# Kernel optimization log

Measured on AMD Instinct MI355X. Metric: run time of the kernel, lower is better.

## Reference

```python
import jax, jax.numpy as jnp
import numpy as np

HIDDEN = 4096


def setup_inputs() -> dict:
    key = jax.random.key(0)
    k1, k2 = jax.random.split(key)
    hidden_states = jax.random.normal(k1, (8, 2048, HIDDEN), dtype=jnp.float32)
    # gate_proj ~ N(0, 0.02^2), shape (2*hidden, hidden)
    gate_proj = 0.02 * jax.random.normal(k2, (2 * HIDDEN, HIDDEN), dtype=jnp.float32)
    return {"hidden_states": hidden_states, "gate_proj": gate_proj, "world_size": 8}


def reference(hidden_states, gate_proj, world_size):
    h = gate_proj.shape[1]
    view = hidden_states.reshape(-1, h)                 # [N, h]
    mm = jnp.einsum("nh,oh->no", view, gate_proj)      # [N, 2h]  (x @ W.T)
    n, o = mm.shape
    # reduce-scatter over dim 0 with world_size ranks: sum the per-rank chunks
    out = mm.reshape(world_size, n // world_size, o).sum(axis=0)  # [N/W, 2h]
    return out
```

## Files before the change

kernel.cpp:

```cpp
#include <hip/hip_runtime.h>
#include <hip/hip_bf16.h>


#define HID   4096
#define SEQ   2048
#define WORLD 8
#define OUTD  8192

typedef __bf16 bf16x8 __attribute__((ext_vector_type(8)));
typedef short  s16x8  __attribute__((ext_vector_type(8)));
typedef float  f32x4  __attribute__((ext_vector_type(4)));

typedef const __attribute__((address_space(1))) void* gas1_ptr;
typedef __attribute__((address_space(3))) void*       las3_ptr;

static __device__ __forceinline__ unsigned short f2bf(float f) {
    union { float f; unsigned u; } v; v.f = f;
    unsigned u = v.u;
    u += 0x7fffu + ((u >> 16) & 1u);
    return (unsigned short)(u >> 16);
}

__global__ void reduce_x_kernel(const float* __restrict__ hs,
                                unsigned short* __restrict__ xb) {
    const int total4 = SEQ * HID / 4;
    const float4* h4 = (const float4*)hs;
    ushort4* o4 = (ushort4*)xb;
    for (int i = blockIdx.x * blockDim.x + threadIdx.x; i < total4;
         i += gridDim.x * blockDim.x) {
        float4 s = h4[i];
        #pragma unroll
        for (int w = 1; w < WORLD; ++w) {
            float4 t = h4[i + w * total4];
            s.x += t.x; s.y += t.y; s.z += t.z; s.w += t.w;
        }
        ushort4 o;
        o.x = f2bf(s.x); o.y = f2bf(s.y); o.z = f2bf(s.z); o.w = f2bf(s.w);
        o4[i] = o;
    }
}

__global__ void convert_w_kernel(const float* __restrict__ w,
                                 unsigned short* __restrict__ wb) {
    const int total4 = OUTD * HID / 4;
    const float4* w4 = (const float4*)w;
    ushort4* o4 = (ushort4*)wb;
    for (int i = blockIdx.x * blockDim.x + threadIdx.x; i < total4;
         i += gridDim.x * blockDim.x) {
        float4 s = w4[i];
        ushort4 o;
        o.x = f2bf(s.x); o.y = f2bf(s.y); o.z = f2bf(s.z); o.w = f2bf(s.w);
        o4[i] = o;
    }
}


#define BM 256
#define BN 256
#define BK 64
#define KSTEPS (HID / BK)

__global__ __launch_bounds__(512, 2)
void gemm_bt_kernel(const unsigned short* __restrict__ A,
                    const unsigned short* __restrict__ B,
                    float* __restrict__ C) {
    __shared__ __align__(16) unsigned short lsA[2][BM * BK];
    __shared__ __align__(16) unsigned short lsB[2][BN * BK];

    const int tid  = threadIdx.x;
    const int lane = tid & 63;
    const int wave = tid >> 6;
    const int wm   = wave >> 2;
    const int wn   = wave & 3;

    const int bid    = blockIdx.x;
    const int tileid = (bid & 7) * 32 + (bid >> 3);
    const int bm = tileid >> 5;
    const int bn = tileid & 31;

    const int subrow = lane >> 3;
    const int slot   = lane & 7;
    const int scol   = (slot ^ subrow) * 8;
    const unsigned short* aBase =
        A + (size_t)(bm * BM + wave * 8 + subrow) * HID + scol;
    const unsigned short* bBase =
        B + (size_t)(bn * BN + wave * 8 + subrow) * HID + scol;
    const int ldsW = wave * 8 * BK;

#define ST_A(buf, ktv, l) __builtin_amdgcn_global_load_lds(                     \
        (gas1_ptr)(aBase + (size_t)(ktv) * BK + (size_t)(l) * 64 * HID),        \
        (las3_ptr)(&lsA[buf][(l) * 64 * BK + ldsW]), 16, 0, 0)
#define ST_B(buf, ktv, l) __builtin_amdgcn_global_load_lds(                     \
        (gas1_ptr)(bBase + (size_t)(ktv) * BK + (size_t)(l) * 64 * HID),        \
        (las3_ptr)(&lsB[buf][(l) * 64 * BK + ldsW]), 16, 0, 0)

    const int fr    = lane & 15;
    const int fq    = lane >> 4;
    const int axor  = fr & 7;
    const int koff0 = ((0 + fq) ^ axor) * 8;
    const int koff1 = ((4 + fq) ^ axor) * 8;
    const int aRowB = (wm * 128 + fr) * BK;
    const int bRowB = (wn * 64 + fr) * BK;

#define RD_A(dst, p, mm, koff) dst = __builtin_bit_cast(bf16x8,                 \
        *(const s16x8*)&lsA[p][aRowB + (mm) * 16 * BK + (koff)])
#define RD_B(dst, p, nn, koff) dst = __builtin_bit_cast(bf16x8,                 \
        *(const s16x8*)&lsB[p][bRowB + (nn) * 16 * BK + (koff)])

#define BARRIER() __builtin_amdgcn_s_barrier()
#define LGKM0()   asm volatile("s_waitcnt lgkmcnt(0)" ::: "memory")
#define VMC4()    asm volatile("s_waitcnt vmcnt(4)" ::: "memory")
#define VMC0()    asm volatile("s_waitcnt vmcnt(0)" ::: "memory")
#define PRIO1()   __builtin_amdgcn_s_setprio(1)
#define PRIO0()   __builtin_amdgcn_s_setprio(0)

    f32x4 acc[8][4] = {};
    bf16x8 va[4][2], vb[4][2];

    ST_A(0, 0, 0); ST_A(0, 0, 1); ST_A(0, 0, 2); ST_A(0, 0, 3);
    ST_B(0, 0, 0); ST_B(0, 0, 1); ST_B(0, 0, 2); ST_B(0, 0, 3);
    ST_A(1, 1, 0); ST_A(1, 1, 1); ST_A(1, 1, 2); ST_A(1, 1, 3);
    VMC4();
    BARRIER();

    for (int kt = 0; kt < KSTEPS; ++kt) {
        const int p = kt & 1;
        const int q = p ^ 1;
        const bool s1 = (kt + 1 < KSTEPS);
        const bool s2 = (kt + 2 < KSTEPS);

        RD_A(va[0][0], p, 0, koff0); RD_A(va[0][1], p, 0, koff1);
        RD_A(va[1][0], p, 1, koff0); RD_A(va[1][1], p, 1, koff1);
        RD_A(va[2][0], p, 2, koff0); RD_A(va[2][1], p, 2, koff1);
        RD_A(va[3][0], p, 3, koff0); RD_A(va[3][1], p, 3, koff1);
        RD_B(vb[0][0], p, 0, koff0); RD_B(vb[0][1], p, 0, koff1);
        RD_B(vb[1][0], p, 1, koff0); RD_B(vb[1][1], p, 1, koff1);
        if (s1) { ST_B(q, kt + 1, 0); ST_B(q, kt + 1, 1); }
        BARRIER();
        LGKM0();
        PRIO1();
        #pragma unroll
        for (int s = 0; s < 2; ++s)
            #pragma unroll
            for (int m = 0; m < 4; ++m)
                #pragma unroll
                for (int n = 0; n < 2; ++n)
                    acc[m][n] = __builtin_amdgcn_mfma_f32_16x16x32_bf16(
                        va[m][s], vb[n][s], acc[m][n], 0, 0, 0);
        PRIO0();
        BARRIER();

        RD_B(vb[2][0], p, 2, koff0); RD_B(vb[2][1], p, 2, koff1);
        RD_B(vb[3][0], p, 3, koff0); RD_B(vb[3][1], p, 3, koff1);
        if (s1) { ST_B(q, kt + 1, 2); ST_B(q, kt + 1, 3); }
        BARRIER();
        LGKM0();
        PRIO1();
        #pragma unroll
        for (int s = 0; s < 2; ++s)
            #pragma unroll
            for (int m = 0; m < 4; ++m)
                #pragma unroll
                for (int n = 0; n < 2; ++n)
                    acc[m][2 + n] = __builtin_amdgcn_mfma_f32_16x16x32_bf16(
                        va[m][s], vb[2 + n][s], acc[m][2 + n], 0, 0, 0);
        PRIO0();
        BARRIER();

        RD_A(va[0][0], p, 4, koff0); RD_A(va[0][1], p, 4, koff1);
        RD_A(va[1][0], p, 5, koff0); RD_A(va[1][1], p, 5, koff1);
        RD_A(va[2][0], p, 6, koff0); RD_A(va[2][1], p, 6, koff1);
        RD_A(va[3][0], p, 7, koff0); RD_A(va[3][1], p, 7, koff1);
        BARRIER();
        LGKM0();
        PRIO1();
        #pragma unroll
        for (int s = 0; s < 2; ++s)
            #pragma unroll
            for (int m = 0; m < 4; ++m)
                #pragma unroll
                for (int n = 0; n < 2; ++n)
                    acc[4 + m][n] = __builtin_amdgcn_mfma_f32_16x16x32_bf16(
                        va[m][s], vb[n][s], acc[4 + m][n], 0, 0, 0);
        PRIO0();
        BARRIER();

        if (s2) { ST_A(p, kt + 2, 0); ST_A(p, kt + 2, 1);
                  ST_A(p, kt + 2, 2); ST_A(p, kt + 2, 3); }
        BARRIER();
        PRIO1();
        #pragma unroll
        for (int s = 0; s < 2; ++s)
            #pragma unroll
            for (int m = 0; m < 4; ++m)
                #pragma unroll
                for (int n = 0; n < 2; ++n)
                    acc[4 + m][2 + n] = __builtin_amdgcn_mfma_f32_16x16x32_bf16(
                        va[m][s], vb[2 + n][s], acc[4 + m][2 + n], 0, 0, 0);
        PRIO0();
        if (s2) { VMC4(); } else { VMC0(); }
        BARRIER();
    }

    const long crow0 = (long)bm * BM + wm * 128 + fq * 4;
    const long ccol0 = (long)bn * BN + wn * 64 + fr;
    #pragma unroll
    for (int m = 0; m < 8; ++m)
        #pragma unroll
        for (int n = 0; n < 4; ++n)
            #pragma unroll
            for (int j = 0; j < 4; ++j)
                C[(crow0 + m * 16 + j) * OUTD + ccol0 + n * 16] = acc[m][n][j];
}

extern "C" void kernel_launch(void* const* d_in, const int* in_sizes, int n_in,
                              void* d_out, int out_size, void* d_ws, size_t ws_size,
                              hipStream_t stream) {
    const float* hs = (const float*)d_in[0];
    const float* w  = (const float*)d_in[1];
    float* out = (float*)d_out;

    unsigned short* xb = (unsigned short*)d_ws;
    unsigned short* wb = xb + (size_t)SEQ * HID;

    hipLaunchKernelGGL(reduce_x_kernel, dim3(2048), dim3(256), 0, stream, hs, xb);
    hipLaunchKernelGGL(convert_w_kernel, dim3(4096), dim3(256), 0, stream, w, wb);
    hipLaunchKernelGGL(gemm_bt_kernel, dim3((SEQ / BM) * (OUTD / BN)), dim3(512),
                       0, stream, xb, wb, out);
}
```

Baseline: 242.0 us.

## Merge prep kernels, remap tiles per XCD, prefetch B two stages ahead

The separate reduce and convert kernels are merged into one launch that splits its blocks between the two jobs, removing one launch and the gap between kernels. The GEMM maps tiles so that each XCD gets a contiguous 4x8 block of output tiles, which should improve L2 reuse of A and B rows. The main loop now reads all four B fragments up front, iterates over A in pairs of rows, and issues both the A and B global-to-LDS loads two k-steps ahead with a vmcnt(8) wait. The deeper prefetch hides more memory latency but keeps more loads in flight and changes register pressure.

```diff
diff --git a/kernel.cpp b/kernel.cpp
--- a/kernel.cpp
+++ b/kernel.cpp
@@ -21,36 +21,39 @@
     return (unsigned short)(u >> 16);
 }
 
-__global__ void reduce_x_kernel(const float* __restrict__ hs,
-                                unsigned short* __restrict__ xb) {
-    const int total4 = SEQ * HID / 4;
-    const float4* h4 = (const float4*)hs;
-    ushort4* o4 = (ushort4*)xb;
-    for (int i = blockIdx.x * blockDim.x + threadIdx.x; i < total4;
-         i += gridDim.x * blockDim.x) {
-        float4 s = h4[i];
-        #pragma unroll
-        for (int w = 1; w < WORLD; ++w) {
-            float4 t = h4[i + w * total4];
-            s.x += t.x; s.y += t.y; s.z += t.z; s.w += t.w;
+#define RED_BLOCKS  2048
+#define CONV_BLOCKS 4096
+__global__ void prep_kernel(const float* __restrict__ hs,
+                            const float* __restrict__ w,
+                            unsigned short* __restrict__ xb,
+                            unsigned short* __restrict__ wb) {
+    if (blockIdx.x < RED_BLOCKS) {
+        const int total4 = SEQ * HID / 4;
+        const float4* h4 = (const float4*)hs;
+        ushort4* o4 = (ushort4*)xb;
+        for (int i = blockIdx.x * blockDim.x + threadIdx.x; i < total4;
+             i += RED_BLOCKS * blockDim.x) {
+            float4 s = h4[i];
+            #pragma unroll
+            for (int ww = 1; ww < WORLD; ++ww) {
+                float4 t = h4[i + ww * total4];
+                s.x += t.x; s.y += t.y; s.z += t.z; s.w += t.w;
+            }
+            ushort4 o;
+            o.x = f2bf(s.x); o.y = f2bf(s.y); o.z = f2bf(s.z); o.w = f2bf(s.w);
+            o4[i] = o;
         }
-        ushort4 o;
-        o.x = f2bf(s.x); o.y = f2bf(s.y); o.z = f2bf(s.z); o.w = f2bf(s.w);
-        o4[i] = o;
-    }
-}
-
-__global__ void convert_w_kernel(const float* __restrict__ w,
-                                 unsigned short* __restrict__ wb) {
-    const int total4 = OUTD * HID / 4;
-    const float4* w4 = (const float4*)w;
-    ushort4* o4 = (ushort4*)wb;
-    for (int i = blockIdx.x * blockDim.x + threadIdx.x; i < total4;
-         i += gridDim.x * blockDim.x) {
-        float4 s = w4[i];
-        ushort4 o;
-        o.x = f2bf(s.x); o.y = f2bf(s.y); o.z = f2bf(s.z); o.w = f2bf(s.w);
-        o4[i] = o;
+    } else {
+        const int total4 = OUTD * HID / 4;
+        const float4* w4 = (const float4*)w;
+        ushort4* o4 = (ushort4*)wb;
+        for (int i = (blockIdx.x - RED_BLOCKS) * blockDim.x + threadIdx.x;
+             i < total4; i += CONV_BLOCKS * blockDim.x) {
+            float4 s = w4[i];
+            ushort4 o;
+            o.x = f2bf(s.x); o.y = f2bf(s.y); o.z = f2bf(s.z); o.w = f2bf(s.w);
+            o4[i] = o;
+        }
     }
 }
 
@@ -73,10 +76,11 @@
     const int wm   = wave >> 2;
     const int wn   = wave & 3;
 
-    const int bid    = blockIdx.x;
-    const int tileid = (bid & 7) * 32 + (bid >> 3);
-    const int bm = tileid >> 5;
-    const int bn = tileid & 31;
+    const int bid   = blockIdx.x;
+    const int xcd   = bid & 7;
+    const int local = bid >> 3;
+    const int bm = (xcd >> 2) * 4 + (local >> 3);
+    const int bn = (xcd & 3) * 8 + (local & 7);
 
     const int subrow = lane >> 3;
     const int slot   = lane & 7;
@@ -109,96 +113,95 @@
 
 #define BARRIER() __builtin_amdgcn_s_barrier()
 #define LGKM0()   asm volatile("s_waitcnt lgkmcnt(0)" ::: "memory")
-#define VMC4()    asm volatile("s_waitcnt vmcnt(4)" ::: "memory")
+#define VMC8()    asm volatile("s_waitcnt vmcnt(8)" ::: "memory")
 #define VMC0()    asm volatile("s_waitcnt vmcnt(0)" ::: "memory")
 #define PRIO1()   __builtin_amdgcn_s_setprio(1)
 #define PRIO0()   __builtin_amdgcn_s_setprio(0)
 
     f32x4 acc[8][4] = {};
-    bf16x8 va[4][2], vb[4][2];
+    bf16x8 va[2][2], va2[2][2], vb[4][2];
 
     ST_A(0, 0, 0); ST_A(0, 0, 1); ST_A(0, 0, 2); ST_A(0, 0, 3);
     ST_B(0, 0, 0); ST_B(0, 0, 1); ST_B(0, 0, 2); ST_B(0, 0, 3);
     ST_A(1, 1, 0); ST_A(1, 1, 1); ST_A(1, 1, 2); ST_A(1, 1, 3);
-    VMC4();
+    ST_B(1, 1, 0); ST_B(1, 1, 1); ST_B(1, 1, 2); ST_B(1, 1, 3);
+    VMC8();
     BARRIER();
 
     for (int kt = 0; kt < KSTEPS; ++kt) {
         const int p = kt & 1;
-        const int q = p ^ 1;
-        const bool s1 = (kt + 1 < KSTEPS);
-        const bool s2 = (kt + 2 < KSTEPS);
-
+        const bool st = (kt + 2 < KSTEPS);
+
+        RD_B(vb[0][0], p, 0, koff0); RD_B(vb[0][1], p, 0, koff1);
+        RD_B(vb[1][0], p, 1, koff0); RD_B(vb[1][1], p, 1, koff1);
+        RD_B(vb[2][0], p, 2, koff0); RD_B(vb[2][1], p, 2, koff1);
+        RD_B(vb[3][0], p, 3, koff0); RD_B(vb[3][1], p, 3, koff1);
         RD_A(va[0][0], p, 0, koff0); RD_A(va[0][1], p, 0, koff1);
         RD_A(va[1][0], p, 1, koff0); RD_A(va[1][1], p, 1, koff1);
-        RD_A(va[2][0], p, 2, koff0); RD_A(va[2][1], p, 2, koff1);
-        RD_A(va[3][0], p, 3, koff0); RD_A(va[3][1], p, 3, koff1);
-        RD_B(vb[0][0], p, 0, koff0); RD_B(vb[0][1], p, 0, koff1);
-        RD_B(vb[1][0], p, 1, koff0); RD_B(vb[1][1], p, 1, koff1);
-        if (s1) { ST_B(q, kt + 1, 0); ST_B(q, kt + 1, 1); }
         BARRIER();
         LGKM0();
         PRIO1();
         #pragma unroll
         for (int s = 0; s < 2; ++s)
             #pragma unroll
-            for (int m = 0; m < 4; ++m)
-                #pragma unroll
-                for (int n = 0; n < 2; ++n)
+            for (int m = 0; m < 2; ++m)
+                #pragma unroll
+                for (int n = 0; n < 4; ++n)
                     acc[m][n] = __builtin_amdgcn_mfma_f32_16x16x32_bf16(
                         va[m][s], vb[n][s], acc[m][n], 0, 0, 0);
         PRIO0();
         BARRIER();
 
-        RD_B(vb[2][0], p, 2, koff0); RD_B(vb[2][1], p, 2, koff1);
-        RD_B(vb[3][0], p, 3, koff0); RD_B(vb[3][1], p, 3, koff1);
-        if (s1) { ST_B(q, kt + 1, 2); ST_B(q, kt + 1, 3); }
+        RD_A(va[0][0], p, 2, koff0); RD_A(va[0][1], p, 2, koff1);
+        RD_A(va[1][0], p, 3, koff0); RD_A(va[1][1], p, 3, koff1);
+        if (st) { ST_B(p, kt + 2, 0); ST_B(p, kt + 2, 1);
+                  ST_B(p, kt + 2, 2); ST_B(p, kt + 2, 3); }
         BARRIER();
         LGKM0();
         PRIO1();
         #pragma unroll
         for (int s = 0; s < 2; ++s)
             #pragma unroll
-            for (int m = 0; m < 4; ++m)
-                #pragma unroll
-                for (int n = 0; n < 2; ++n)
-                    acc[m][2 + n] = __builtin_amdgcn_mfma_f32_16x16x32_bf16(
-                        va[m][s], vb[2 + n][s], acc[m][2 + n], 0, 0, 0);
-        PRIO0();
-        BARRIER();
-
-        RD_A(va[0][0], p, 4, koff0); RD_A(va[0][1], p, 4, koff1);
-        RD_A(va[1][0], p, 5, koff0); RD_A(va[1][1], p, 5, koff1);
-        RD_A(va[2][0], p, 6, koff0); RD_A(va[2][1], p, 6, koff1);
-        RD_A(va[3][0], p, 7, koff0); RD_A(va[3][1], p, 7, koff1);
+            for (int m = 0; m < 2; ++m)
+                #pragma unroll
+                for (int n = 0; n < 4; ++n)
+                    acc[2 + m][n] = __builtin_amdgcn_mfma_f32_16x16x32_bf16(
+                        va[m][s], vb[n][s], acc[2 + m][n], 0, 0, 0);
+        PRIO0();
+        BARRIER();
+
+        RD_A(va[0][0],  p, 4, koff0); RD_A(va[0][1],  p, 4, koff1);
+        RD_A(va[1][0],  p, 5, koff0); RD_A(va[1][1],  p, 5, koff1);
+        RD_A(va2[0][0], p, 6, koff0); RD_A(va2[0][1], p, 6, koff1);
+        RD_A(va2[1][0], p, 7, koff0); RD_A(va2[1][1], p, 7, koff1);
         BARRIER();
         LGKM0();
         PRIO1();
         #pragma unroll
         for (int s = 0; s < 2; ++s)
             #pragma unroll
-            for (int m = 0; m < 4; ++m)
-                #pragma unroll
-                for (int n = 0; n < 2; ++n)
+            for (int m = 0; m < 2; ++m)
+                #pragma unroll
+                for (int n = 0; n < 4; ++n)
                     acc[4 + m][n] = __builtin_amdgcn_mfma_f32_16x16x32_bf16(
                         va[m][s], vb[n][s], acc[4 + m][n], 0, 0, 0);
         PRIO0();
         BARRIER();
 
-        if (s2) { ST_A(p, kt + 2, 0); ST_A(p, kt + 2, 1);
+        if (st) { ST_A(p, kt + 2, 0); ST_A(p, kt + 2, 1);
                   ST_A(p, kt + 2, 2); ST_A(p, kt + 2, 3); }
         BARRIER();
         PRIO1();
         #pragma unroll
         for (int s = 0; s < 2; ++s)
             #pragma unroll
-            for (int m = 0; m < 4; ++m)
-                #pragma unroll
-                for (int n = 0; n < 2; ++n)
-                    acc[4 + m][2 + n] = __builtin_amdgcn_mfma_f32_16x16x32_bf16(
-                        va[m][s], vb[2 + n][s], acc[4 + m][2 + n], 0, 0, 0);
-        PRIO0();
-        if (s2) { VMC4(); } else { VMC0(); }
+            for (int m = 0; m < 2; ++m)
+                #pragma unroll
+                for (int n = 0; n < 4; ++n)
+                    acc[6 + m][n] = __builtin_amdgcn_mfma_f32_16x16x32_bf16(
+                        va2[m][s], vb[n][s], acc[6 + m][n], 0, 0, 0);
+        PRIO0();
+        if (st) { VMC8(); } else { VMC0(); }
         BARRIER();
     }
 
@@ -223,8 +226,8 @@
     unsigned short* xb = (unsigned short*)d_ws;
     unsigned short* wb = xb + (size_t)SEQ * HID;
 
-    hipLaunchKernelGGL(reduce_x_kernel, dim3(2048), dim3(256), 0, stream, hs, xb);
-    hipLaunchKernelGGL(convert_w_kernel, dim3(4096), dim3(256), 0, stream, w, wb);
+    hipLaunchKernelGGL(prep_kernel, dim3(RED_BLOCKS + CONV_BLOCKS), dim3(256),
+                       0, stream, hs, w, xb, wb);
     hipLaunchKernelGGL(gemm_bt_kernel, dim3((SEQ / BM) * (OUTD / BN)), dim3(512),
                        0, stream, xb, wb, out);
 }
```

Measured after the change: 235.1 us. 1.03x faster.
